# Performance work log

Measured on AMD Instinct MI355X. Metric: run time of the kernel, lower is better.

## Reference

```python
import jax, jax.numpy as jnp
import numpy as np

S, B, H, L = 1024, 128, 1024, 2
D = 2 * H  # concat dim: hidden + input (input_size == hidden_size)


def setup_inputs() -> dict:
    key = jax.random.key(0)
    k1, k2, k3 = jax.random.split(key, 3)
    inputs = jax.random.normal(k1, (S, B, H), dtype=jnp.float32)
    lim = 1.0 / np.sqrt(D)  # torch Linear default init range
    W = jax.random.uniform(k2, (L, 4, D), jnp.float32, -lim, lim)  # rows: i, c~, f, o
    b = jax.random.uniform(k3, (L, 4), jnp.float32, -lim, lim)
    return {"inputs": inputs, "W": W, "b": b}


def _lstm(inputs, W, b):
    Ln = W.shape[0]
    Bn, Hd = inputs.shape[1], inputs.shape[2]
    h0 = jnp.zeros((Ln, Bn, Hd), inputs.dtype)
    c0 = jnp.zeros_like(h0)

    def step(carry, x_t):
        h, c = carry  # each [L, B, H]
        inp = x_t     # [B, H]
        hs, cs = [], []
        for l in range(Ln):
            z = jnp.concatenate([h[l], inp], axis=-1)  # [B, 2H], order [H_t_1, X_t]
            g = z @ W[l].T + b[l]                       # [B, 4] — four 1-out Linears fused
            i_t = jax.nn.sigmoid(g[:, 0:1])
            c_hat = jnp.tanh(g[:, 1:2])
            f_t = jax.nn.sigmoid(g[:, 2:3])
            o_t = jax.nn.sigmoid(g[:, 3:4])
            c_new = f_t * c[l] + i_t * c_hat            # scalar gates broadcast over [B, H]
            h_new = o_t * jnp.tanh(c_new)
            hs.append(h_new)
            cs.append(c_new)
            inp = h_new
        h = jnp.stack(hs)
        c = jnp.stack(cs)
        return (h, c), h[-1]

    (hT, cT), outs = jax.lax.scan(step, (h0, c0), inputs)
    return outs, hT, cT  # outs: [S, B, H]


def reference(inputs, W, b):
    outs, hT, cT = _lstm(inputs, W, b)
    return (outs, (hT, cT))
```

## Files before the change

### kernel.cpp

```cpp
#include <hip/hip_runtime.h>

#define SS 1024
#define BB 128
#define HH 1024
#define DD 2048
#define NROWS (SS*BB)
#define NSEG 16
#define TSEG 64
#define ROWSEG (TSEG*BB)
#define NSCANB 4
#define NK1B   512
#define NK3B   504
#define NBLK   (NSCANB+NK1B+NK3B)
#define K1WAVES 2048
#define L2E  1.4426950408889634f
#define PF 16

#define K1FLAG(s,sh) (((s)*8 + (sh))*32)
#define SCFLAG(s)    (4096 + (s)*32)
#define FLAG_INTS    4608

typedef float f32x4 __attribute__((ext_vector_type(4)));

__device__ __forceinline__ float fast_rcp(float x)  { return __builtin_amdgcn_rcpf(x); }
__device__ __forceinline__ float exp2_(float x)     { return __builtin_amdgcn_exp2f(x); }

__device__ __forceinline__ void st_wt(float* p, float v){
    asm volatile("global_store_dword %0, %1, off sc0 sc1" :: "v"(p), "v"(v));
}
__device__ __forceinline__ void st_wt_x4(float* p, f32x4 v){
    asm volatile("global_store_dwordx4 %0, %1, off sc0 sc1" :: "v"(p), "v"(v));
}

template<int CTRL>
__device__ __forceinline__ float qperm(float x){
    return __int_as_float(__builtin_amdgcn_update_dpp(0, __float_as_int(x), CTRL, 0xF, 0xF, true));
}
__device__ __forceinline__ float rowshr4(float x){
    return __int_as_float(__builtin_amdgcn_update_dpp(0, __float_as_int(x), 0x114, 0xF, 0xF, true));
}

__global__ __launch_bounds__(256, 4) void lstm_df(
    const float* __restrict__ x, const float* __restrict__ W,
    const float* __restrict__ bias, float* out,
    float* __restrict__ s_out, float* __restrict__ finals,
    int* __restrict__ flags)
{
    __shared__ int ready;
    float* pre = out + (size_t)NROWS * HH;
    const int tid  = threadIdx.x;
    const int lane = tid & 63;
    const int wv   = tid >> 6;
    const int blk  = blockIdx.x;

    if (blk < NSCANB) {
        const int sw   = blk*4 + wv;
        const int gate = lane & 3;
        const int L    = (lane >> 2) & 1;
        const int lb   = lane >> 3;
        const int bb   = sw*8 + lb;

        float sh = 0.f, sx = 0.f;
        for (int q = 0; q < 12; ++q) {
            const int base = (q < 4) ? q*DD
                           : (q < 8) ? 4*DD + (q-4)*DD
                                     : 4*DD + (q-8)*DD + HH;
            float v = 0.f;
            #pragma unroll
            for (int k = 0; k < 16; ++k) v += W[base + lane + k*64];
            #pragma unroll
            for (int off = 32; off >= 1; off >>= 1) v += __shfl_xor(v, off, 64);
            if (q == L*4 + gate) sh = v;
            if (q == 8 + gate)   sx = v;
        }
        const float sc  = (gate == 1) ? (2.0f*L2E) : (-L2E);
        const float s_h = sh * sc;
        const float sxc = L ? sx * sc : 0.0f;
        const float pcc = L ? bias[4+gate] * sc : 0.0f;
        const float Ac  = (gate == 1) ? 1.0f : 0.0f;
        const float Bc  = (gate == 0) ? (2.0f*L2E) : ((gate == 1) ? -2.0f : 1.0f);

        const float* pbase = pre + ((size_t)bb << 12) + gate;
        float* obase = s_out + bb;

        float h = 0.f, cp = 0.f, h0d1 = 0.f, h0d2 = 0.f;

        for (int s = 0; s < NSEG; ++s) {
            {
                int guard = 0;
                for (;;) {
                    int tot = 0;
                    #pragma unroll
                    for (int i = 0; i < 8; ++i)
                        tot += __hip_atomic_load(&flags[K1FLAG(s,i)], __ATOMIC_RELAXED, __HIP_MEMORY_SCOPE_AGENT);
                    if (tot >= K1WAVES) break;
                    __builtin_amdgcn_s_sleep(8);
                    if (++guard > (1<<20)) break;
                }
                asm volatile("" ::: "memory");
            }
            const int t_lo = s*TSEG, t_hi = t_lo + TSEG;
            float buf[PF];
            #pragma unroll
            for (int u = 0; u < PF; ++u)
                buf[u] = __builtin_nontemporal_load(pbase + (size_t)(t_lo + u) * 4);

            for (int t0 = t_lo; t0 < t_hi; t0 += PF) {
                #pragma unroll
                for (int u = 0; u < PF; ++u) {
                    const int t = t0 + u;
                    const float p = L ? pcc : buf[u];
                    int tn = t + PF; if (tn > t_hi-1) tn = t_hi-1;
                    buf[u] = __builtin_nontemporal_load(pbase + (size_t)tn * 4);

                    const float P = fmaf(h0d2, sxc, p);
                    const float g = fmaf(h, s_h, P);
                    const float v = fmaf(Bc, fast_rcp(1.0f + exp2_(g)), Ac);
                    const float w = v * qperm<0xB1>(v);
                    const float cpn = fmaf(qperm<0xAA>(v), cp, qperm<0x00>(w));
                    const float th = fmaf(-2.0f, fast_rcp(1.0f + exp2_(cpn)), 1.0f);
                    const float hn = qperm<0xFF>(v) * th;
                    const bool disc = (u < 2) && (t0 == t_lo) && L;
                    h  = disc ? h  : hn;
                    cp = disc ? cp : cpn;
                    h0d2 = h0d1;
                    h0d1 = rowshr4(h);
                    if (L && t >= t_lo + 2)
                        st_wt(obase + (size_t)(t-2) * BB, h);
                }
            }

            const float h0f = h, c0f = cp;

            #pragma unroll
            for (int fs = 0; fs < 2; ++fs) {
                const float p = L ? pcc : buf[0];
                const float P = fmaf(h0d2, sxc, p);
                const float g = fmaf(h, s_h, P);
                const float v = fmaf(Bc, fast_rcp(1.0f + exp2_(g)), Ac);
                const float w = v * qperm<0xB1>(v);
                const float cpn = fmaf(qperm<0xAA>(v), cp, qperm<0x00>(w));
                const float th = fmaf(-2.0f, fast_rcp(1.0f + exp2_(cpn)), 1.0f);
                const float hn = qperm<0xFF>(v) * th;
                if (L) { h = hn; cp = cpn;
                         st_wt(obase + (size_t)(t_hi-2+fs) * BB, hn); }
                h0d2 = h0d1;
            }

            if (s == NSEG-1 && gate == 0) {
                if (L) { st_wt(finals + 128 + bb, h);
                         st_wt(finals + 384 + bb, cp  * (0.5f/L2E)); }
                else   { st_wt(finals + bb,       h0f);
                         st_wt(finals + 256 + bb, c0f * (0.5f/L2E)); }
            }

            asm volatile("s_waitcnt vmcnt(0)" ::: "memory");
            if (lane == 0)
                __hip_atomic_fetch_add(&flags[SCFLAG(s)], 1, __ATOMIC_RELAXED, __HIP_MEMORY_SCOPE_AGENT);
        }
        return;
    }

    if (blk < NSCANB + NK1B) {
        const int i = (blk - NSCANB)*4 + wv;
        float4 wvv[4][4];
        #pragma unroll
        for (int j = 0; j < 4; ++j)
            #pragma unroll
            for (int it = 0; it < 4; ++it)
                wvv[j][it] = *(const float4*)(W + j*DD + HH + it*256 + lane*4);
        const float4 b0 = *(const float4*)(bias);

        for (int s = 0; s < NSEG; ++s) {
            #pragma unroll 2
            for (int j = 0; j < 4; ++j) {
                const int row = s*ROWSEG + i*4 + j;
                const float* xr = x + (size_t)row * HH;
                float a0 = 0.f, a1 = 0.f, a2 = 0.f, a3 = 0.f;
                #pragma unroll
                for (int it = 0; it < 4; ++it) {
                    f32x4 xv = __builtin_nontemporal_load((const f32x4*)xr + it*64 + lane);
                    a0 = fmaf(xv.x, wvv[0][it].x, fmaf(xv.y, wvv[0][it].y, fmaf(xv.z, wvv[0][it].z, fmaf(xv.w, wvv[0][it].w, a0))));
                    a1 = fmaf(xv.x, wvv[1][it].x, fmaf(xv.y, wvv[1][it].y, fmaf(xv.z, wvv[1][it].z, fmaf(xv.w, wvv[1][it].w, a1))));
                    a2 = fmaf(xv.x, wvv[2][it].x, fmaf(xv.y, wvv[2][it].y, fmaf(xv.z, wvv[2][it].z, fmaf(xv.w, wvv[2][it].w, a2))));
                    a3 = fmaf(xv.x, wvv[3][it].x, fmaf(xv.y, wvv[3][it].y, fmaf(xv.z, wvv[3][it].z, fmaf(xv.w, wvv[3][it].w, a3))));
                }
                #pragma unroll
                for (int off = 32; off >= 1; off >>= 1) {
                    a0 += __shfl_xor(a0, off, 64);
                    a1 += __shfl_xor(a1, off, 64);
                    a2 += __shfl_xor(a2, off, 64);
                    a3 += __shfl_xor(a3, off, 64);
                }
                if (lane == 0) {
                    const int b = row & (BB-1), t = row >> 7;
                    f32x4 r = {(a0 + b0.x) * (-L2E),
                               (a1 + b0.y) * ( 2.0f * L2E),
                               (a2 + b0.z) * (-L2E),
                               (a3 + b0.w) * (-L2E)};
                    st_wt_x4(pre + (((size_t)b << 10) + t) * 4, r);
                }
            }
            asm volatile("s_waitcnt vmcnt(0)" ::: "memory");
            if (lane == 0)
                __hip_atomic_fetch_add(&flags[K1FLAG(s, i & 7)], 1, __ATOMIC_RELAXED, __HIP_MEMORY_SCOPE_AGENT);
        }
        return;
    }

    if (tid == 0) ready = 0;
    __syncthreads();
    const int u = (blk - NSCANB - NK1B)*4 + wv;
    const int lbase = (u < 32) ? u*8 : 256 + (u-32)*4;
    const int cnt   = (u < 32) ? 8 : 4;
    for (int s = 0; s < NSEG; ++s) {
        if (tid == 0) {
            int guard = 0;
            while (__hip_atomic_load(&flags[SCFLAG(s)], __ATOMIC_RELAXED, __HIP_MEMORY_SCOPE_AGENT) < 16) {
                __builtin_amdgcn_s_sleep(32);
                if (++guard > (1<<19)) break;
            }
            __hip_atomic_store(&ready, s+1, __ATOMIC_RELAXED, __HIP_MEMORY_SCOPE_WORKGROUP);
        }
        {
            int guard = 0;
            while (__hip_atomic_load(&ready, __ATOMIC_RELAXED, __HIP_MEMORY_SCOPE_WORKGROUP) < s+1) {
                __builtin_amdgcn_s_sleep(4);
                if (++guard > (1<<22)) break;
            }
            asm volatile("" ::: "memory");
        }
        const int r0 = s*ROWSEG + lbase;
        for (int q = 0; q < cnt; q += 4) {
            f32x4 v4 = __builtin_nontemporal_load((const f32x4*)(s_out + r0 + q));
            #pragma unroll
            for (int jj = 0; jj < 4; ++jj) {
                const float vb = (jj==0) ? v4.x : (jj==1) ? v4.y : (jj==2) ? v4.z : v4.w;
                const f32x4 vv = {vb, vb, vb, vb};
                f32x4* dst = (f32x4*)(out + (size_t)(r0 + q + jj) * HH);
                #pragma unroll
                for (int it = 0; it < 4; ++it)
                    __builtin_nontemporal_store(vv, dst + it*64 + lane);
            }
        }
    }
    if (u < 512) {
        const float v = __builtin_nontemporal_load(finals + u);
        const f32x4 vv = {v, v, v, v};
        f32x4* dst = (f32x4*)(out + (size_t)(NROWS + u) * HH);
        #pragma unroll
        for (int it = 0; it < 4; ++it)
            __builtin_nontemporal_store(vv, dst + it*64 + lane);
    }
}

extern "C" void kernel_launch(void* const* d_in, const int* in_sizes, int n_in,
                              void* d_out, int out_size, void* d_ws, size_t ws_size,
                              hipStream_t stream) {
    const float* x    = (const float*)d_in[0];
    const float* W    = (const float*)d_in[1];
    const float* bias = (const float*)d_in[2];
    float* out = (float*)d_out;

    float* s_out  = (float*)d_ws;
    float* finals = s_out + NROWS;
    int*   flags  = (int*)(finals + 512);

    hipMemsetAsync(flags, 0, FLAG_INTS * sizeof(int), stream);
    hipLaunchKernelGGL(lstm_df, dim3(NBLK), dim3(256), 0, stream,
                       x, W, bias, out, s_out, finals, flags);
}
```

Before: 279.3 us.

## Transpose pre-activation and scan-output layouts for batched segment loads and vector stores

Changes the pre-activation buffer layout to per-batch, per-segment, per-gate contiguous runs, so each scan lane loads a whole 64-step segment with sixteen dwordx4 loads up front instead of a rolling 16-deep prefetch of strided scalar loads. The scan output is now stored time-contiguous per batch, and only gate-0 lanes write it, batched four steps at a time as dwordx4 write-through stores. The producer now writes four scalar stores from four lanes, and the broadcast blocks remap their indices to read the new layout. The intent is to take load latency and store traffic off the serial recurrence critical path, at the cost of more registers and a full wait before each segment starts.

```diff
diff --git a/kernel.cpp b/kernel.cpp
--- a/kernel.cpp
+++ b/kernel.cpp
@@ -14,7 +14,6 @@
 #define NBLK   (NSCANB+NK1B+NK3B)
 #define K1WAVES 2048
 #define L2E  1.4426950408889634f
-#define PF 16
 
 #define K1FLAG(s,sh) (((s)*8 + (sh))*32)
 #define SCFLAG(s)    (4096 + (s)*32)
@@ -80,10 +79,11 @@
         const float Ac  = (gate == 1) ? 1.0f : 0.0f;
         const float Bc  = (gate == 0) ? (2.0f*L2E) : ((gate == 1) ? -2.0f : 1.0f);
 
-        const float* pbase = pre + ((size_t)bb << 12) + gate;
-        float* obase = s_out + bb;
+        const float* pcol = pre + ((size_t)bb << 12) + gate*TSEG;
+        float* so = s_out + (size_t)bb * SS;
 
         float h = 0.f, cp = 0.f, h0d1 = 0.f, h0d2 = 0.f;
+        float hb0 = 0.f, hb1 = 0.f, hb2 = 0.f, hb3 = 0.f;
 
         for (int s = 0; s < NSEG; ++s) {
             {
@@ -100,33 +100,40 @@
                 asm volatile("" ::: "memory");
             }
             const int t_lo = s*TSEG, t_hi = t_lo + TSEG;
-            float buf[PF];
-            #pragma unroll
-            for (int u = 0; u < PF; ++u)
-                buf[u] = __builtin_nontemporal_load(pbase + (size_t)(t_lo + u) * 4);
-
-            for (int t0 = t_lo; t0 < t_hi; t0 += PF) {
-                #pragma unroll
-                for (int u = 0; u < PF; ++u) {
-                    const int t = t0 + u;
-                    const float p = L ? pcc : buf[u];
-                    int tn = t + PF; if (tn > t_hi-1) tn = t_hi-1;
-                    buf[u] = __builtin_nontemporal_load(pbase + (size_t)tn * 4);
-
-                    const float P = fmaf(h0d2, sxc, p);
-                    const float g = fmaf(h, s_h, P);
-                    const float v = fmaf(Bc, fast_rcp(1.0f + exp2_(g)), Ac);
-                    const float w = v * qperm<0xB1>(v);
-                    const float cpn = fmaf(qperm<0xAA>(v), cp, qperm<0x00>(w));
-                    const float th = fmaf(-2.0f, fast_rcp(1.0f + exp2_(cpn)), 1.0f);
-                    const float hn = qperm<0xFF>(v) * th;
-                    const bool disc = (u < 2) && (t0 == t_lo) && L;
-                    h  = disc ? h  : hn;
-                    cp = disc ? cp : cpn;
-                    h0d2 = h0d1;
-                    h0d1 = rowshr4(h);
-                    if (L && t >= t_lo + 2)
-                        st_wt(obase + (size_t)(t-2) * BB, h);
+
+            const float* pb = pcol + s*256;
+            f32x4 sv[16];
+            #pragma unroll
+            for (int q = 0; q < 16; ++q)
+                asm volatile("global_load_dwordx4 %0, %1, off offset:%2"
+                             : "=v"(sv[q]) : "v"(pb), "i"(q*16));
+            asm volatile("s_waitcnt vmcnt(0)" ::: "memory");
+            __builtin_amdgcn_sched_barrier(0);
+
+            #pragma unroll
+            for (int u = 0; u < TSEG; ++u) {
+                const float p = L ? pcc : sv[u>>2][u&3];
+
+                const float P = fmaf(h0d2, sxc, p);
+                const float g = fmaf(h, s_h, P);
+                const float v = fmaf(Bc, fast_rcp(1.0f + exp2_(g)), Ac);
+                const float w = v * qperm<0xB1>(v);
+                const float cpn = fmaf(qperm<0xAA>(v), cp, qperm<0x00>(w));
+                const float th = fmaf(-2.0f, fast_rcp(1.0f + exp2_(cpn)), 1.0f);
+                const float hn = qperm<0xFF>(v) * th;
+                const bool disc = (u < 2) && L;
+                h  = disc ? h  : hn;
+                cp = disc ? cp : cpn;
+                h0d2 = h0d1;
+                h0d1 = rowshr4(h);
+
+                if (((u+2)&3)==0) hb0 = h;
+                else if (((u+2)&3)==1) hb1 = h;
+                else if (((u+2)&3)==2) hb2 = h;
+                else hb3 = h;
+                if ((u&3)==1 && u>=5 && L && gate==0) {
+                    f32x4 hv = {hb0,hb1,hb2,hb3};
+                    st_wt_x4(so + t_lo + u - 5, hv);
                 }
             }
 
@@ -134,7 +141,7 @@
 
             #pragma unroll
             for (int fs = 0; fs < 2; ++fs) {
-                const float p = L ? pcc : buf[0];
+                const float p = L ? pcc : sv[0][0];
                 const float P = fmaf(h0d2, sxc, p);
                 const float g = fmaf(h, s_h, P);
                 const float v = fmaf(Bc, fast_rcp(1.0f + exp2_(g)), Ac);
@@ -143,8 +150,12 @@
                 const float th = fmaf(-2.0f, fast_rcp(1.0f + exp2_(cpn)), 1.0f);
                 const float hn = qperm<0xFF>(v) * th;
                 if (L) { h = hn; cp = cpn;
-                         st_wt(obase + (size_t)(t_hi-2+fs) * BB, hn); }
+                         if (fs == 0) hb2 = hn; else hb3 = hn; }
                 h0d2 = h0d1;
+            }
+            if (L && gate == 0) {
+                f32x4 hv = {hb0,hb1,hb2,hb3};
+                st_wt_x4(so + t_hi - 4, hv);
             }
 
             if (s == NSEG-1 && gate == 0) {
@@ -192,13 +203,14 @@
                     a2 += __shfl_xor(a2, off, 64);
                     a3 += __shfl_xor(a3, off, 64);
                 }
-                if (lane == 0) {
+                if (lane < 4) {
                     const int b = row & (BB-1), t = row >> 7;
-                    f32x4 r = {(a0 + b0.x) * (-L2E),
-                               (a1 + b0.y) * ( 2.0f * L2E),
-                               (a2 + b0.z) * (-L2E),
-                               (a3 + b0.w) * (-L2E)};
-                    st_wt_x4(pre + (((size_t)b << 10) + t) * 4, r);
+                    const float g0 = (a0 + b0.x) * (-L2E);
+                    const float g1 = (a1 + b0.y) * ( 2.0f * L2E);
+                    const float g2 = (a2 + b0.z) * (-L2E);
+                    const float g3 = (a3 + b0.w) * (-L2E);
+                    const float mv = (lane==0) ? g0 : (lane==1) ? g1 : (lane==2) ? g2 : g3;
+                    st_wt(pre + ((size_t)b << 12) + s*256 + lane*TSEG + (t & (TSEG-1)), mv);
                 }
             }
             asm volatile("s_waitcnt vmcnt(0)" ::: "memory");
@@ -211,8 +223,7 @@
     if (tid == 0) ready = 0;
     __syncthreads();
     const int u = (blk - NSCANB - NK1B)*4 + wv;
-    const int lbase = (u < 32) ? u*8 : 256 + (u-32)*4;
-    const int cnt   = (u < 32) ? 8 : 4;
+    const int nrep = (u < 32) ? 2 : 1;
     for (int s = 0; s < NSEG; ++s) {
         if (tid == 0) {
             int guard = 0;
@@ -230,14 +241,16 @@
             }
             asm volatile("" ::: "memory");
         }
-        const int r0 = s*ROWSEG + lbase;
-        for (int q = 0; q < cnt; q += 4) {
-            f32x4 v4 = __builtin_nontemporal_load((const f32x4*)(s_out + r0 + q));
+        for (int rep = 0; rep < nrep; ++rep) {
+            const int g  = rep ? (2016 + u) : u;
+            const int b  = g >> 4;
+            const int t0 = s*TSEG + (g & 15)*4;
+            f32x4 v4 = __builtin_nontemporal_load((const f32x4*)(s_out + (size_t)b*SS + t0));
             #pragma unroll
             for (int jj = 0; jj < 4; ++jj) {
                 const float vb = (jj==0) ? v4.x : (jj==1) ? v4.y : (jj==2) ? v4.z : v4.w;
                 const f32x4 vv = {vb, vb, vb, vb};
-                f32x4* dst = (f32x4*)(out + (size_t)(r0 + q + jj) * HH);
+                f32x4* dst = (f32x4*)(out + ((size_t)(t0+jj)*BB + b) * HH);
                 #pragma unroll
                 for (int it = 0; it < 4; ++it)
                     __builtin_nontemporal_store(vv, dst + it*64 + lane);
```

Result: faster. 247.3 us (-11.5%).

## Split input projection into separate kernel and spread scan over more blocks

Applied to the files above, without the earlier changes.

The single dataflow kernel is split in two. A first kernel computes the full input projection and the weight row sums. A second kernel runs the scan and the broadcast writer, with the scan spread over 16 single-wave blocks and each segment's 64 pre-activations loaded up front. The scan output is now stored batch-major with vectorised x4 writes, and the writer blocks poll with shorter sleeps. This removes the per-segment flag polling between projection and scan, at the cost of losing the overlap between the projection phase and the recurrent scan.

```diff
diff --git a/kernel.cpp b/kernel.cpp
--- a/kernel.cpp
+++ b/kernel.cpp
@@ -5,18 +5,13 @@
 #define HH 1024
 #define DD 2048
 #define NROWS (SS*BB)
+#define TSEG 64
 #define NSEG 16
-#define TSEG 64
-#define ROWSEG (TSEG*BB)
-#define NSCANB 4
-#define NK1B   512
-#define NK3B   504
-#define NBLK   (NSCANB+NK1B+NK3B)
-#define K1WAVES 2048
+#define NSCANB 16
+#define NK3B 512
+#define NBLKB (NSCANB + NK3B)
 #define L2E  1.4426950408889634f
-#define PF 16
-
-#define K1FLAG(s,sh) (((s)*8 + (sh))*32)
+
 #define SCFLAG(s)    (4096 + (s)*32)
 #define FLAG_INTS    4608
 
@@ -40,11 +35,73 @@
     return __int_as_float(__builtin_amdgcn_update_dpp(0, __float_as_int(x), 0x114, 0xF, 0xF, true));
 }
 
-__global__ __launch_bounds__(256, 4) void lstm_df(
+__global__ __launch_bounds__(256) void k1_all(
     const float* __restrict__ x, const float* __restrict__ W,
+    const float* __restrict__ bias, float* out, float* __restrict__ sums)
+{
+    float* pre = out + (size_t)NROWS * HH;
+    const int tid  = threadIdx.x;
+    const int lane = tid & 63;
+    const int wv   = tid >> 6;
+
+    if (blockIdx.x == 0 && tid < 64) {
+        for (int s = 0; s < 12; ++s) {
+            const int base = (s < 4) ? s*DD
+                           : (s < 8) ? 4*DD + (s-4)*DD
+                                     : 4*DD + (s-8)*DD + HH;
+            float v = 0.f;
+            #pragma unroll
+            for (int k = 0; k < 16; ++k) v += W[base + lane + k*64];
+            #pragma unroll
+            for (int off = 32; off >= 1; off >>= 1) v += __shfl_xor(v, off, 64);
+            if (lane == 0) sums[s] = v;
+        }
+    }
+
+    const int gw = blockIdx.x*4 + wv;
+    float4 wvv[4][4];
+    #pragma unroll
+    for (int j = 0; j < 4; ++j)
+        #pragma unroll
+        for (int it = 0; it < 4; ++it)
+            wvv[j][it] = *(const float4*)(W + j*DD + HH + it*256 + lane*4);
+    const float4 b0 = *(const float4*)(bias);
+
+    #pragma unroll 2
+    for (int j = 0; j < 16; ++j) {
+        const int row = gw*16 + j;
+        const float* xr = x + (size_t)row * HH;
+        float a0 = 0.f, a1 = 0.f, a2 = 0.f, a3 = 0.f;
+        #pragma unroll
+        for (int it = 0; it < 4; ++it) {
+            f32x4 xv = __builtin_nontemporal_load((const f32x4*)xr + it*64 + lane);
+            a0 = fmaf(xv.x, wvv[0][it].x, fmaf(xv.y, wvv[0][it].y, fmaf(xv.z, wvv[0][it].z, fmaf(xv.w, wvv[0][it].w, a0))));
+            a1 = fmaf(xv.x, wvv[1][it].x, fmaf(xv.y, wvv[1][it].y, fmaf(xv.z, wvv[1][it].z, fmaf(xv.w, wvv[1][it].w, a1))));
+            a2 = fmaf(xv.x, wvv[2][it].x, fmaf(xv.y, wvv[2][it].y, fmaf(xv.z, wvv[2][it].z, fmaf(xv.w, wvv[2][it].w, a2))));
+            a3 = fmaf(xv.x, wvv[3][it].x, fmaf(xv.y, wvv[3][it].y, fmaf(xv.z, wvv[3][it].z, fmaf(xv.w, wvv[3][it].w, a3))));
+        }
+        #pragma unroll
+        for (int off = 32; off >= 1; off >>= 1) {
+            a0 += __shfl_xor(a0, off, 64);
+            a1 += __shfl_xor(a1, off, 64);
+            a2 += __shfl_xor(a2, off, 64);
+            a3 += __shfl_xor(a3, off, 64);
+        }
+        if (lane == 0) {
+            float4 r = make_float4((a0 + b0.x) * (-L2E),
+                                   (a1 + b0.y) * ( 2.0f * L2E),
+                                   (a2 + b0.z) * (-L2E),
+                                   (a3 + b0.w) * (-L2E));
+            const int b = row & (BB-1), t = row >> 7;
+            *(float4*)(pre + (((size_t)b << 10) + t) * 4) = r;
+        }
+    }
+}
+
+__global__ __launch_bounds__(256, 4) void scan_k3(
     const float* __restrict__ bias, float* out,
     float* __restrict__ s_out, float* __restrict__ finals,
-    int* __restrict__ flags)
+    const float* __restrict__ sums, int* __restrict__ flags)
 {
     __shared__ int ready;
     float* pre = out + (size_t)NROWS * HH;
@@ -54,25 +111,14 @@
     const int blk  = blockIdx.x;
 
     if (blk < NSCANB) {
-        const int sw   = blk*4 + wv;
+        if (wv != 0) return;
         const int gate = lane & 3;
         const int L    = (lane >> 2) & 1;
         const int lb   = lane >> 3;
-        const int bb   = sw*8 + lb;
-
-        float sh = 0.f, sx = 0.f;
-        for (int q = 0; q < 12; ++q) {
-            const int base = (q < 4) ? q*DD
-                           : (q < 8) ? 4*DD + (q-4)*DD
-                                     : 4*DD + (q-8)*DD + HH;
-            float v = 0.f;
-            #pragma unroll
-            for (int k = 0; k < 16; ++k) v += W[base + lane + k*64];
-            #pragma unroll
-            for (int off = 32; off >= 1; off >>= 1) v += __shfl_xor(v, off, 64);
-            if (q == L*4 + gate) sh = v;
-            if (q == 8 + gate)   sx = v;
-        }
+        const int bb   = blk*8 + lb;
+
+        const float sh = sums[L*4 + gate];
+        const float sx = sums[8 + gate];
         const float sc  = (gate == 1) ? (2.0f*L2E) : (-L2E);
         const float s_h = sh * sc;
         const float sxc = L ? sx * sc : 0.0f;
@@ -81,60 +127,49 @@
         const float Bc  = (gate == 0) ? (2.0f*L2E) : ((gate == 1) ? -2.0f : 1.0f);
 
         const float* pbase = pre + ((size_t)bb << 12) + gate;
-        float* obase = s_out + bb;
+        float* so = s_out + (size_t)bb * SS;
 
         float h = 0.f, cp = 0.f, h0d1 = 0.f, h0d2 = 0.f;
+        float hb0 = 0.f, hb1 = 0.f, hb2 = 0.f, hb3 = 0.f;
 
         for (int s = 0; s < NSEG; ++s) {
-            {
-                int guard = 0;
-                for (;;) {
-                    int tot = 0;
-                    #pragma unroll
-                    for (int i = 0; i < 8; ++i)
-                        tot += __hip_atomic_load(&flags[K1FLAG(s,i)], __ATOMIC_RELAXED, __HIP_MEMORY_SCOPE_AGENT);
-                    if (tot >= K1WAVES) break;
-                    __builtin_amdgcn_s_sleep(8);
-                    if (++guard > (1<<20)) break;
+            const int t_lo = s*TSEG, t_hi = t_lo + TSEG;
+            float buf[TSEG];
+            #pragma unroll
+            for (int uu = 0; uu < TSEG; ++uu)
+                buf[uu] = pbase[(size_t)(t_lo + uu) * 4];
+
+            #pragma unroll
+            for (int uu = 0; uu < TSEG; ++uu) {
+                const float p = L ? pcc : buf[uu];
+                const float P = fmaf(h0d2, sxc, p);
+                const float g = fmaf(h, s_h, P);
+                const float v = fmaf(Bc, fast_rcp(1.0f + exp2_(g)), Ac);
+                const float w = v * qperm<0xB1>(v);
+                const float cpn = fmaf(qperm<0xAA>(v), cp, qperm<0x00>(w));
+                const float th = fmaf(-2.0f, fast_rcp(1.0f + exp2_(cpn)), 1.0f);
+                const float hn = qperm<0xFF>(v) * th;
+                const bool disc = (uu < 2) && L;
+                h  = disc ? h  : hn;
+                cp = disc ? cp : cpn;
+                h0d2 = h0d1;
+                h0d1 = rowshr4(h);
+
+                if (((uu+2)&3)==0) hb0 = h;
+                else if (((uu+2)&3)==1) hb1 = h;
+                else if (((uu+2)&3)==2) hb2 = h;
+                else hb3 = h;
+                if (((uu&3)==1) && uu >= 5 && L && gate == 0) {
+                    f32x4 hv = {hb0,hb1,hb2,hb3};
+                    st_wt_x4(so + t_lo + uu - 5, hv);
                 }
-                asm volatile("" ::: "memory");
-            }
-            const int t_lo = s*TSEG, t_hi = t_lo + TSEG;
-            float buf[PF];
-            #pragma unroll
-            for (int u = 0; u < PF; ++u)
-                buf[u] = __builtin_nontemporal_load(pbase + (size_t)(t_lo + u) * 4);
-
-            for (int t0 = t_lo; t0 < t_hi; t0 += PF) {
-                #pragma unroll
-                for (int u = 0; u < PF; ++u) {
-                    const int t = t0 + u;
-                    const float p = L ? pcc : buf[u];
-                    int tn = t + PF; if (tn > t_hi-1) tn = t_hi-1;
-                    buf[u] = __builtin_nontemporal_load(pbase + (size_t)tn * 4);
-
-                    const float P = fmaf(h0d2, sxc, p);
-                    const float g = fmaf(h, s_h, P);
-                    const float v = fmaf(Bc, fast_rcp(1.0f + exp2_(g)), Ac);
-                    const float w = v * qperm<0xB1>(v);
-                    const float cpn = fmaf(qperm<0xAA>(v), cp, qperm<0x00>(w));
-                    const float th = fmaf(-2.0f, fast_rcp(1.0f + exp2_(cpn)), 1.0f);
-                    const float hn = qperm<0xFF>(v) * th;
-                    const bool disc = (u < 2) && (t0 == t_lo) && L;
-                    h  = disc ? h  : hn;
-                    cp = disc ? cp : cpn;
-                    h0d2 = h0d1;
-                    h0d1 = rowshr4(h);
-                    if (L && t >= t_lo + 2)
-                        st_wt(obase + (size_t)(t-2) * BB, h);
-                }
             }
 
             const float h0f = h, c0f = cp;
 
             #pragma unroll
             for (int fs = 0; fs < 2; ++fs) {
-                const float p = L ? pcc : buf[0];
+                const float p = L ? pcc : buf[TSEG-1];
                 const float P = fmaf(h0d2, sxc, p);
                 const float g = fmaf(h, s_h, P);
                 const float v = fmaf(Bc, fast_rcp(1.0f + exp2_(g)), Ac);
@@ -143,8 +178,12 @@
                 const float th = fmaf(-2.0f, fast_rcp(1.0f + exp2_(cpn)), 1.0f);
                 const float hn = qperm<0xFF>(v) * th;
                 if (L) { h = hn; cp = cpn;
-                         st_wt(obase + (size_t)(t_hi-2+fs) * BB, hn); }
+                         if (fs == 0) hb2 = hn; else hb3 = hn; }
                 h0d2 = h0d1;
+            }
+            if (L && gate == 0) {
+                f32x4 hv = {hb0,hb1,hb2,hb3};
+                st_wt_x4(so + t_hi - 4, hv);
             }
 
             if (s == NSEG-1 && gate == 0) {
@@ -161,91 +200,41 @@
         return;
     }
 
-    if (blk < NSCANB + NK1B) {
-        const int i = (blk - NSCANB)*4 + wv;
-        float4 wvv[4][4];
-        #pragma unroll
-        for (int j = 0; j < 4; ++j)
-            #pragma unroll
-            for (int it = 0; it < 4; ++it)
-                wvv[j][it] = *(const float4*)(W + j*DD + HH + it*256 + lane*4);
-        const float4 b0 = *(const float4*)(bias);
-
-        for (int s = 0; s < NSEG; ++s) {
-            #pragma unroll 2
-            for (int j = 0; j < 4; ++j) {
-                const int row = s*ROWSEG + i*4 + j;
-                const float* xr = x + (size_t)row * HH;
-                float a0 = 0.f, a1 = 0.f, a2 = 0.f, a3 = 0.f;
-                #pragma unroll
-                for (int it = 0; it < 4; ++it) {
-                    f32x4 xv = __builtin_nontemporal_load((const f32x4*)xr + it*64 + lane);
-                    a0 = fmaf(xv.x, wvv[0][it].x, fmaf(xv.y, wvv[0][it].y, fmaf(xv.z, wvv[0][it].z, fmaf(xv.w, wvv[0][it].w, a0))));
-                    a1 = fmaf(xv.x, wvv[1][it].x, fmaf(xv.y, wvv[1][it].y, fmaf(xv.z, wvv[1][it].z, fmaf(xv.w, wvv[1][it].w, a1))));
-                    a2 = fmaf(xv.x, wvv[2][it].x, fmaf(xv.y, wvv[2][it].y, fmaf(xv.z, wvv[2][it].z, fmaf(xv.w, wvv[2][it].w, a2))));
-                    a3 = fmaf(xv.x, wvv[3][it].x, fmaf(xv.y, wvv[3][it].y, fmaf(xv.z, wvv[3][it].z, fmaf(xv.w, wvv[3][it].w, a3))));
-                }
-                #pragma unroll
-                for (int off = 32; off >= 1; off >>= 1) {
-                    a0 += __shfl_xor(a0, off, 64);
-                    a1 += __shfl_xor(a1, off, 64);
-                    a2 += __shfl_xor(a2, off, 64);
-                    a3 += __shfl_xor(a3, off, 64);
-                }
-                if (lane == 0) {
-                    const int b = row & (BB-1), t = row >> 7;
-                    f32x4 r = {(a0 + b0.x) * (-L2E),
-                               (a1 + b0.y) * ( 2.0f * L2E),
-                               (a2 + b0.z) * (-L2E),
-                               (a3 + b0.w) * (-L2E)};
-                    st_wt_x4(pre + (((size_t)b << 10) + t) * 4, r);
-                }
-            }
-            asm volatile("s_waitcnt vmcnt(0)" ::: "memory");
-            if (lane == 0)
-                __hip_atomic_fetch_add(&flags[K1FLAG(s, i & 7)], 1, __ATOMIC_RELAXED, __HIP_MEMORY_SCOPE_AGENT);
-        }
-        return;
-    }
-
     if (tid == 0) ready = 0;
     __syncthreads();
-    const int u = (blk - NSCANB - NK1B)*4 + wv;
-    const int lbase = (u < 32) ? u*8 : 256 + (u-32)*4;
-    const int cnt   = (u < 32) ? 8 : 4;
+    const int u = (blk - NSCANB)*4 + wv;
+    const int b = u >> 4;
     for (int s = 0; s < NSEG; ++s) {
         if (tid == 0) {
             int guard = 0;
             while (__hip_atomic_load(&flags[SCFLAG(s)], __ATOMIC_RELAXED, __HIP_MEMORY_SCOPE_AGENT) < 16) {
-                __builtin_amdgcn_s_sleep(32);
-                if (++guard > (1<<19)) break;
+                __builtin_amdgcn_s_sleep(2);
+                if (++guard > (1<<23)) break;
             }
             __hip_atomic_store(&ready, s+1, __ATOMIC_RELAXED, __HIP_MEMORY_SCOPE_WORKGROUP);
         }
         {
             int guard = 0;
             while (__hip_atomic_load(&ready, __ATOMIC_RELAXED, __HIP_MEMORY_SCOPE_WORKGROUP) < s+1) {
-                __builtin_amdgcn_s_sleep(4);
-                if (++guard > (1<<22)) break;
+                __builtin_amdgcn_s_sleep(1);
+                if (++guard > (1<<24)) break;
             }
             asm volatile("" ::: "memory");
         }
-        const int r0 = s*ROWSEG + lbase;
-        for (int q = 0; q < cnt; q += 4) {
-            f32x4 v4 = __builtin_nontemporal_load((const f32x4*)(s_out + r0 + q));
-            #pragma unroll
-            for (int jj = 0; jj < 4; ++jj) {
-                const float vb = (jj==0) ? v4.x : (jj==1) ? v4.y : (jj==2) ? v4.z : v4.w;
-                const f32x4 vv = {vb, vb, vb, vb};
-                f32x4* dst = (f32x4*)(out + (size_t)(r0 + q + jj) * HH);
-                #pragma unroll
-                for (int it = 0; it < 4; ++it)
-                    __builtin_nontemporal_store(vv, dst + it*64 + lane);
-            }
+        const int t0 = s*TSEG + (u & 15)*4;
+        float4 v4 = *(const float4*)(s_out + (size_t)b*SS + t0);
+        #pragma unroll
+        for (int jj = 0; jj < 4; ++jj) {
+            const float vb = (jj==0) ? v4.x : (jj==1) ? v4.y : (jj==2) ? v4.z : v4.w;
+            const f32x4 vv = {vb, vb, vb, vb};
+            f32x4* dst = (f32x4*)(out + ((size_t)(t0+jj)*BB + b) * HH);
+            #pragma unroll
+            for (int it = 0; it < 4; ++it)
+                __builtin_nontemporal_store(vv, dst + it*64 + lane);
         }
     }
     if (u < 512) {
-        const float v = __builtin_nontemporal_load(finals + u);
+        const float v = finals[u];
         const f32x4 vv = {v, v, v, v};
         f32x4* dst = (f32x4*)(out + (size_t)(NROWS + u) * HH);
         #pragma unroll
@@ -264,9 +253,12 @@
 
     float* s_out  = (float*)d_ws;
     float* finals = s_out + NROWS;
-    int*   flags  = (int*)(finals + 512);
+    float* sums   = finals + 512;
+    int*   flags  = (int*)(sums + 16);
 
     hipMemsetAsync(flags, 0, FLAG_INTS * sizeof(int), stream);
-    hipLaunchKernelGGL(lstm_df, dim3(NBLK), dim3(256), 0, stream,
-                       x, W, bias, out, s_out, finals, flags);
-}
+    hipLaunchKernelGGL(k1_all, dim3(2048), dim3(256), 0, stream,
+                       x, W, bias, out, sums);
+    hipLaunchKernelGGL(scan_k3, dim3(NBLKB), dim3(256), 0, stream,
+                       bias, out, s_out, finals, sums, flags);
+}
```

New measurement: 252.6 us. 1.11x faster.
